# Optimization experiments

Measured on AMD Instinct MI355X. Metric: run time of the kernel, lower is better.

## Reference

```python
import jax, jax.numpy as jnp
import numpy as np

B, H, W, C = 32, 56, 56, 256
HEADS, WS, SS, MLP = 8, 7, 3, 1024
N = WS * WS          # tokens per window = 49
HD = C // HEADS      # head dim = 32
SCALE = HD ** -0.5
EPS = 1e-5


def _rel_pos_index():
    coords = np.stack(np.meshgrid(np.arange(WS), np.arange(WS), indexing='ij')).reshape(2, -1)
    rel = (coords[:, :, None] - coords[:, None, :]).transpose(1, 2, 0)
    rel[:, :, 0] += WS - 1
    rel[:, :, 1] += WS - 1
    rel[:, :, 0] *= 2 * WS - 1
    return rel.sum(-1)  # (49, 49) int


def _shift_mask():
    ma = np.zeros((H, W), np.float32)
    sl = (slice(0, -WS), slice(-WS, -SS), slice(-SS, None))
    cnt = 0
    for hs in sl:
        for ws_ in sl:
            ma[hs, ws_] = cnt
            cnt += 1
    mw = ma.reshape(H // WS, WS, W // WS, WS).transpose(0, 2, 1, 3).reshape(-1, N)
    diff = mw[:, None, :] - mw[:, :, None]
    return np.where(diff != 0, np.float32(-100.0), np.float32(0.0))  # (nW, 49, 49)


_RPI = _rel_pos_index()
_MASK = jnp.asarray(_shift_mask())


def _ln(x, g, b):
    mu = jnp.mean(x, -1, keepdims=True)
    var = jnp.mean(jnp.square(x - mu), -1, keepdims=True)
    return (x - mu) * jax.lax.rsqrt(var + EPS) * g + b


def setup_inputs() -> dict:
    key = jax.random.key(0)
    ks = jax.random.split(key, 6)
    s = 0.02
    return {
        'x': jax.random.normal(ks[0], (B, H * W, C), jnp.float32),
        'qkv_w': jax.random.normal(ks[1], (C, 3 * C), jnp.float32) * s,
        'qkv_b': jnp.zeros((3 * C,), jnp.float32),
        'proj_w': jax.random.normal(ks[2], (C, C), jnp.float32) * s,
        'proj_b': jnp.zeros((C,), jnp.float32),
        'rel_bias': jax.random.normal(ks[3], ((2 * WS - 1) ** 2, HEADS), jnp.float32) * s,
        'ln1_g': jnp.ones((C,), jnp.float32),
        'ln1_b': jnp.zeros((C,), jnp.float32),
        'ln2_g': jnp.ones((C,), jnp.float32),
        'ln2_b': jnp.zeros((C,), jnp.float32),
        'mlp_w1': jax.random.normal(ks[4], (C, MLP), jnp.float32) * s,
        'mlp_b1': jnp.zeros((MLP,), jnp.float32),
        'mlp_w2': jax.random.normal(ks[5], (MLP, C), jnp.float32) * s,
        'mlp_b2': jnp.zeros((C,), jnp.float32),
    }


def reference(x, qkv_w, qkv_b, proj_w, proj_b, rel_bias,
              ln1_g, ln1_b, ln2_g, ln2_b, mlp_w1, mlp_b1, mlp_w2, mlp_b2):
    b = x.shape[0]
    nW = (H // WS) * (W // WS)

    x_skip = x
    xn = _ln(x, ln1_g, ln1_b).reshape(b, H, W, C)
    shifted = jnp.roll(xn, (-SS, -SS), axis=(1, 2))
    # window partition -> (b*nW, N, C)
    xw = shifted.reshape(b, H // WS, WS, W // WS, WS, C)
    xw = xw.transpose(0, 1, 3, 2, 4, 5).reshape(-1, N, C)

    qkv = (xw @ qkv_w + qkv_b).reshape(-1, N, 3, HEADS, HD).transpose(2, 0, 3, 1, 4)
    q, k, v = qkv[0] * SCALE, qkv[1], qkv[2]  # (b*nW, heads, N, hd)

    attn = jnp.einsum('bhnd,bhmd->bhnm', q, k)
    bias = rel_bias[_RPI.reshape(-1)].reshape(N, N, HEADS).transpose(2, 0, 1)
    attn = attn + bias[None]
    attn = attn.reshape(b, nW, HEADS, N, N) + _MASK[None, :, None]
    attn = jax.nn.softmax(attn.reshape(-1, HEADS, N, N), axis=-1)

    out = jnp.einsum('bhnm,bhmd->bhnd', attn, v)
    out = out.transpose(0, 2, 1, 3).reshape(-1, N, C)
    out = out @ proj_w + proj_b

    # window reverse -> (b, H, W, C)
    out = out.reshape(b, H // WS, W // WS, WS, WS, C)
    out = out.transpose(0, 1, 3, 2, 4, 5).reshape(b, H, W, C)
    out = jnp.roll(out, (SS, SS), axis=(1, 2)).reshape(b, H * W, C)

    x = x_skip + out
    x_skip2 = x
    xn2 = _ln(x, ln2_g, ln2_b)
    h = jax.nn.gelu(xn2 @ mlp_w1 + mlp_b1, approximate=False)
    h = h @ mlp_w2 + mlp_b2
    return x_skip2 + h
```

## Files before the change

### kernel.cpp

```cpp
#include <hip/hip_runtime.h>


typedef unsigned short u16;
typedef __attribute__((ext_vector_type(8))) short bfrag8;
typedef __attribute__((ext_vector_type(8))) unsigned short u16x8;
typedef __attribute__((ext_vector_type(4))) float f32x4;

#define WS_TOK 49
#define C_DIM 256
#define M_ROWS 100352
#define N_WIN 2048
#define SCALE_Q 0.17677669529663689f

#if defined(__has_builtin)
#  if __has_builtin(__builtin_amdgcn_global_load_lds)
#    define HAVE_GLL 1
#  endif
#endif
#ifndef HAVE_GLL
#  define HAVE_GLL 0
#endif

__device__ __forceinline__ float u2f(u16 u) {
    union { unsigned int i; float f; } c; c.i = ((unsigned int)u) << 16; return c.f;
}
__device__ __forceinline__ u16 f2u(float f) {
    union { float f; unsigned int i; } c; c.f = f;
    unsigned int i = c.i;
    return (u16)((i + 0x7fffu + ((i >> 16) & 1u)) >> 16);
}
__device__ __forceinline__ int regionOf(int h) {
    return h < 49 ? 0 : (h < 53 ? 1 : 2);
}
__device__ __forceinline__ float gelu_fast(float v) {
    const float v2 = v * v;
    const float u = v * __builtin_fmaf(-0.0713548162f, v2, -1.5957691216f);
    const float e = __expf(u);
    return v * __builtin_amdgcn_rcpf(1.f + e);
}

__device__ __forceinline__ void g2l16(const u16* g, u16* l) {
#if HAVE_GLL
    __builtin_amdgcn_global_load_lds((const __attribute__((address_space(1))) void*)g,
                                     (__attribute__((address_space(3))) void*)l, 16, 0, 0);
#else
    *(bfrag8*)l = *(const bfrag8*)g;
#endif
}

__global__ void transpose_k(const float* __restrict__ in, u16* __restrict__ out,
                            int R, int Ccols) {
    int i = blockIdx.x * 256 + threadIdx.x;
    if (i < R * Ccols) {
        int r = i / Ccols, c = i - r * Ccols;
        out[(size_t)c * R + r] = f2u(in[i]);
    }
}

__global__ __launch_bounds__(256) void ln_kernel(const float* __restrict__ xin,
                                                 const float* __restrict__ g,
                                                 const float* __restrict__ b,
                                                 u16* __restrict__ out, int mode) {
    const int w = threadIdx.x >> 6, lane = threadIdx.x & 63;
    const int r = blockIdx.x * 4 + w;
    int s = r;
    if (mode == 0) {
        const int win = r / WS_TOK, tok = r - win * WS_TOK;
        const int b_ = win >> 6, w64 = win & 63;
        const int wr = w64 >> 3, wc = w64 & 7;
        const int th = tok / 7, tw = tok - th * 7;
        int hh = wr * 7 + th + 3; if (hh >= 56) hh -= 56;
        int ww = wc * 7 + tw + 3; if (ww >= 56) ww -= 56;
        s = b_ * 3136 + hh * 56 + ww;
    }
    const float4 u = *(const float4*)(xin + (size_t)s * C_DIM + lane * 4);
    float f0 = u.x, f1 = u.y, f2 = u.z, f3 = u.w;
    float s1 = f0 + f1 + f2 + f3;
    float s2 = f0 * f0 + f1 * f1 + f2 * f2 + f3 * f3;
#pragma unroll
    for (int off = 32; off; off >>= 1) {
        s1 += __shfl_xor(s1, off, 64);
        s2 += __shfl_xor(s2, off, 64);
    }
    const float mu = s1 * (1.f / 256.f);
    const float rs = rsqrtf(s2 * (1.f / 256.f) - mu * mu + 1e-5f);
    const float4 ug = *(const float4*)(g + lane * 4);
    const float4 ub = *(const float4*)(b + lane * 4);
    ushort4 o;
    o.x = f2u((f0 - mu) * rs * ug.x + ub.x);
    o.y = f2u((f1 - mu) * rs * ug.y + ub.y);
    o.z = f2u((f2 - mu) * rs * ug.z + ub.z);
    o.w = f2u((f3 - mu) * rs * ug.w + ub.w);
    *(ushort4*)(out + (size_t)r * C_DIM + lane * 4) = o;
}

template <int KD, int ND, int NY, int EPI>
__global__ __launch_bounds__(256) void gemm_bt(const u16* __restrict__ A,
                                               const u16* __restrict__ Bt,
                                               const float* __restrict__ bias,
                                               u16* __restrict__ o0,
                                               u16* __restrict__ o1,
                                               u16* __restrict__ o2,
                                               float* __restrict__ fo,
                                               const float* __restrict__ res) {
    __shared__ __align__(16) char pool[17408];
    u16* As = (u16*)pool;
    u16* Bs = (u16*)(pool + 8192);
    const int tid = threadIdx.x;
    const int bid = blockIdx.x;
    const int m0 = (bid / NY) * 128;
    const int n0 = (bid % NY) * 128;
    const int wid = tid >> 6, lane = tid & 63;
    const int wy = wid >> 1, wx = wid & 1;
    const int l15 = lane & 15, lsel = lane >> 4;

    f32x4 acc[4][4] = {};
    const u16* Ag = A + (size_t)m0 * KD;
    const u16* Bg = Bt + (size_t)n0 * KD;

    for (int k0 = 0; k0 < KD; k0 += 32) {
#pragma unroll
        for (int p = 0; p < 2; ++p) {
            const int idx = p * 256 + tid;
            const int row = idx >> 2, ks = (idx & 3) << 3;
            g2l16(Ag + (size_t)row * KD + k0 + ks, As + idx * 8);
            g2l16(Bg + (size_t)row * KD + k0 + ks, Bs + idx * 8);
        }
        __syncthreads();
        bfrag8 af[4], bfv[4];
#pragma unroll
        for (int m = 0; m < 4; ++m)
            af[m] = *(const bfrag8*)(As + (wy * 64 + m * 16 + l15) * 32 + lsel * 8);
#pragma unroll
        for (int n = 0; n < 4; ++n)
            bfv[n] = *(const bfrag8*)(Bs + (wx * 64 + n * 16 + l15) * 32 + lsel * 8);
#pragma unroll
        for (int m = 0; m < 4; ++m)
#pragma unroll
            for (int n = 0; n < 4; ++n)
                acc[m][n] = __builtin_amdgcn_mfma_f32_16x16x32_bf16(af[m], bfv[n],
                                                                    acc[m][n], 0, 0, 0);
        __syncthreads();
    }

    float* Ts = (float*)pool + wid * (16 * 68);
    const int r  = lane >> 2;
    const int cg = (lane & 3) << 4;

#pragma unroll
    for (int m = 0; m < 4; ++m) {
#pragma unroll
        for (int n = 0; n < 4; ++n)
#pragma unroll
            for (int reg = 0; reg < 4; ++reg)
                Ts[(lsel * 4 + reg) * 68 + n * 16 + l15] = acc[m][n][reg];
        float vals[16];
#pragma unroll
        for (int j = 0; j < 4; ++j)
            *(f32x4*)(vals + 4 * j) = *(const f32x4*)(Ts + r * 68 + cg + 4 * j);

        const int gr  = m0 + wy * 64 + m * 16 + r;
        const int gc0 = n0 + wx * 64 + cg;
        float bias16[16];
#pragma unroll
        for (int j = 0; j < 4; ++j)
            *(f32x4*)(bias16 + 4 * j) = *(const f32x4*)(bias + gc0 + 4 * j);

        if (EPI == 0) {
            const int win = gr / WS_TOK, tok = gr - win * WS_TOK;
            const int part = gc0 >> 8, head = (gc0 >> 5) & 7, hd = gc0 & 31;
            u16* dst = (part == 0) ? o0 : (part == 1) ? o1 : o2;
            const float sc = (part == 0) ? SCALE_Q : 1.f;
            const size_t di = (size_t)win * 8 * (WS_TOK * 32) + (size_t)tok * 32 +
                              (size_t)head * (WS_TOK * 32) + hd;
            u16x8 pk[2];
#pragma unroll
            for (int j = 0; j < 16; ++j)
                ((u16*)pk)[j] = f2u((vals[j] + bias16[j]) * sc);
            *(u16x8*)(dst + di)     = pk[0];
            *(u16x8*)(dst + di + 8) = pk[1];
        } else if (EPI == 1) {
            const int win = gr / WS_TOK, tok = gr - win * WS_TOK;
            const int b_ = win >> 6, w64 = win & 63;
            const int wr = w64 >> 3, wc = w64 & 7;
            const int th = tok / 7, tw = tok - th * 7;
            int hh = wr * 7 + th + 3; if (hh >= 56) hh -= 56;
            int ww = wc * 7 + tw + 3; if (ww >= 56) ww -= 56;
            const size_t di = ((size_t)b_ * 3136 + hh * 56 + ww) * C_DIM + gc0;
#pragma unroll
            for (int j = 0; j < 4; ++j) {
                f32x4 rr = *(const f32x4*)(res + di + 4 * j);
                f32x4 o;
#pragma unroll
                for (int e = 0; e < 4; ++e)
                    o[e] = rr[e] + vals[4 * j + e] + bias16[4 * j + e];
                *(f32x4*)(fo + di + 4 * j) = o;
            }
        } else if (EPI == 2) {
            u16x8 pk[2];
#pragma unroll
            for (int j = 0; j < 16; ++j)
                ((u16*)pk)[j] = f2u(gelu_fast(vals[j] + bias16[j]));
            u16* dst = o0 + (size_t)gr * ND + gc0;
            *(u16x8*)dst       = pk[0];
            *(u16x8*)(dst + 8) = pk[1];
        } else {
            const size_t di = (size_t)gr * ND + gc0;
#pragma unroll
            for (int j = 0; j < 4; ++j) {
                f32x4 rr = *(const f32x4*)(res + di + 4 * j);
                f32x4 o;
#pragma unroll
                for (int e = 0; e < 4; ++e)
                    o[e] = rr[e] + vals[4 * j + e] + bias16[4 * j + e];
                *(f32x4*)(fo + di + 4 * j) = o;
            }
        }
    }
}

__device__ __forceinline__ void stage_w1t(const u16* __restrict__ w1T, u16* dst,
                                          int kc, int k0, int tid) {
#pragma unroll
    for (int p = 0; p < 4; ++p) {
        const int i = p * 256 + tid;
        const int row = i >> 3, s = i & 7;
        g2l16(w1T + (size_t)(kc * 128 + row) * 256 + k0 + ((s ^ (row & 7)) << 3),
              dst + i * 8);
    }
}
__device__ __forceinline__ void stage_w2t(const u16* __restrict__ w2T, u16* dst,
                                          int kc, int bs, int tid) {
#pragma unroll
    for (int p = 0; p < 4; ++p) {
        const int i = p * 256 + tid;
        const int row = i >> 2, s = i & 3;
        g2l16(w2T + (size_t)row * 1024 + kc * 128 + bs * 32 +
                  ((s ^ ((row >> 1) & 3)) << 3),
              dst + i * 8);
    }
}

__global__ __launch_bounds__(256, 2) void fused_mlp(const u16* __restrict__ z,
                                                    const u16* __restrict__ w1T,
                                                    const float* __restrict__ b1,
                                                    const u16* __restrict__ w2T,
                                                    const float* __restrict__ b2,
                                                    float* __restrict__ out) {
    __shared__ __align__(16) u16 pool[40960];
    u16* zS  = pool;
    u16* wb0 = pool + 16384;
    u16* wb1 = pool + 24576;
    u16* hc  = pool + 32768;
    const int tid = threadIdx.x;
    const int wid = tid >> 6, lane = tid & 63;
    const int wy = wid >> 1, wx = wid & 1;
    const int l15 = lane & 15, lsel = lane >> 4;
    const int m0 = blockIdx.x * 64;

#pragma unroll
    for (int p = 0; p < 8; ++p) {
        const int i = p * 256 + tid;
        const int row = i >> 5, s = i & 31;
        g2l16(z + (size_t)(m0 + row) * 256 + ((s ^ (row & 7)) << 3), zS + i * 8);
    }
    stage_w1t(w1T, wb0, 0, 0, tid);

    f32x4 acc2[2][8] = {};

    for (int kc = 0; kc < 8; ++kc) {
        float b1v[4];
#pragma unroll
        for (int n = 0; n < 4; ++n)
            b1v[n] = b1[kc * 128 + wx * 64 + n * 16 + l15];
        asm volatile("" ::: "memory");

        f32x4 acc1[2][4] = {};
#pragma unroll
        for (int ks = 0; ks < 4; ++ks) {
            u16* wc = (ks & 1) ? wb1 : wb0;
            u16* wn = (ks & 1) ? wb0 : wb1;
            if (ks < 3) stage_w1t(w1T, wn, kc, (ks + 1) * 64, tid);
            else        stage_w2t(w2T, wn, kc, 0, tid);
            asm volatile("s_waitcnt vmcnt(4)" ::: "memory");
            __builtin_amdgcn_sched_barrier(0);
            __builtin_amdgcn_s_barrier();
            bfrag8 af[2], bf[4];
#pragma unroll
            for (int m = 0; m < 2; ++m) {
                const int r = wy * 32 + m * 16 + l15;
                af[m] = *(const bfrag8*)(zS + r * 256 +
                         ((ks * 64 + lsel * 8) ^ ((r & 7) << 3)));
            }
#pragma unroll
            for (int n = 0; n < 4; ++n) {
                const int r = wx * 64 + n * 16 + l15;
                bf[n] = *(const bfrag8*)(wc + r * 64 +
                         ((lsel * 8) ^ ((r & 7) << 3)));
            }
            bfrag8 af2[2], bf2[4];
#pragma unroll
            for (int m = 0; m < 2; ++m) {
                const int r = wy * 32 + m * 16 + l15;
                af2[m] = *(const bfrag8*)(zS + r * 256 +
                          ((ks * 64 + 32 + lsel * 8) ^ ((r & 7) << 3)));
            }
#pragma unroll
            for (int n = 0; n < 4; ++n) {
                const int r = wx * 64 + n * 16 + l15;
                bf2[n] = *(const bfrag8*)(wc + r * 64 +
                          ((32 + lsel * 8) ^ ((r & 7) << 3)));
            }
            __builtin_amdgcn_s_setprio(1);
#pragma unroll
            for (int m = 0; m < 2; ++m)
#pragma unroll
                for (int n = 0; n < 4; ++n)
                    acc1[m][n] = __builtin_amdgcn_mfma_f32_16x16x32_bf16(
                        af[m], bf[n], acc1[m][n], 0, 0, 0);
#pragma unroll
            for (int m = 0; m < 2; ++m)
#pragma unroll
                for (int n = 0; n < 4; ++n)
                    acc1[m][n] = __builtin_amdgcn_mfma_f32_16x16x32_bf16(
                        af2[m], bf2[n], acc1[m][n], 0, 0, 0);
            __builtin_amdgcn_s_setprio(0);
            if (ks == 3) {
#pragma unroll
                for (int m = 0; m < 2; ++m)
#pragma unroll
                    for (int n = 0; n < 4; ++n)
#pragma unroll
                        for (int reg = 0; reg < 4; ++reg) {
                            const int rh = wy * 32 + m * 16 + lsel * 4 + reg;
                            const int ch = wx * 64 + n * 16 + l15;
                            hc[rh * 128 + (ch ^ ((rh & 15) << 3))] =
                                f2u(gelu_fast(acc1[m][n][reg] + b1v[n]));
                        }
                asm volatile("s_waitcnt lgkmcnt(0)" ::: "memory");
                __builtin_amdgcn_sched_barrier(0);
            }
            __builtin_amdgcn_s_barrier();
        }
#pragma unroll
        for (int bs = 0; bs < 4; ++bs) {
            u16* wc = (bs & 1) ? wb1 : wb0;
            u16* wn = (bs & 1) ? wb0 : wb1;
            if (bs < 3)      stage_w2t(w2T, wn, kc, bs + 1, tid);
            else if (kc < 7) stage_w1t(w1T, wn, kc + 1, 0, tid);
            if (bs == 3 && kc == 7) asm volatile("s_waitcnt vmcnt(0)" ::: "memory");
            else                    asm volatile("s_waitcnt vmcnt(4)" ::: "memory");
            __builtin_amdgcn_sched_barrier(0);
            __builtin_amdgcn_s_barrier();
            bfrag8 a2[2], bb[8];
#pragma unroll
            for (int m = 0; m < 2; ++m) {
                const int r = wy * 32 + m * 16 + l15;
                a2[m] = *(const bfrag8*)(hc + r * 128 +
                         ((bs * 32 + lsel * 8) ^ ((r & 15) << 3)));
            }
#pragma unroll
            for (int n = 0; n < 8; ++n) {
                const int r = wx * 128 + n * 16 + l15;
                bb[n] = *(const bfrag8*)(wc + r * 32 +
                         ((lsel * 8) ^ (((r >> 1) & 3) << 3)));
            }
            __builtin_amdgcn_s_setprio(1);
#pragma unroll
            for (int m = 0; m < 2; ++m)
#pragma unroll
                for (int n = 0; n < 8; ++n)
                    acc2[m][n] = __builtin_amdgcn_mfma_f32_16x16x32_bf16(
                        a2[m], bb[n], acc2[m][n], 0, 0, 0);
            __builtin_amdgcn_s_setprio(0);
            __builtin_amdgcn_s_barrier();
        }
    }

    float* Ts = (float*)pool + wid * (16 * 132);
    const int r  = lane >> 2;
    const int cg = (lane & 3) << 5;
#pragma unroll
    for (int m = 0; m < 2; ++m) {
#pragma unroll
        for (int n = 0; n < 8; ++n)
#pragma unroll
            for (int reg = 0; reg < 4; ++reg)
                Ts[(lsel * 4 + reg) * 132 + n * 16 + l15] = acc2[m][n][reg];
        float vals[32];
#pragma unroll
        for (int j = 0; j < 8; ++j)
            *(f32x4*)(vals + 4 * j) = *(const f32x4*)(Ts + r * 132 + cg + 4 * j);

        const int gr = m0 + wy * 32 + m * 16 + r;
        const size_t dbase = (size_t)gr * 256 + wx * 128 + cg;
#pragma unroll
        for (int j = 0; j < 8; ++j) {
            f32x4 rr = *(const f32x4*)(out + dbase + 4 * j);
            f32x4 bb4 = *(const f32x4*)(b2 + wx * 128 + cg + 4 * j);
            f32x4 o;
#pragma unroll
            for (int e = 0; e < 4; ++e)
                o[e] = rr[e] + vals[4 * j + e] + bb4[e];
            *(f32x4*)(out + dbase + 4 * j) = o;
        }
    }
}

__global__ __launch_bounds__(256) void attn_kernel(const u16* __restrict__ q,
                                                   const u16* __restrict__ k,
                                                   const u16* __restrict__ v,
                                                   const float* __restrict__ relb,
                                                   u16* __restrict__ ao) {
    __shared__ __align__(16) u16 PbAll[4][64 * 64];
    __shared__ __align__(16) u16 VtAll[4][32 * 64];
    const int wid = threadIdx.x >> 6;
    const int lane = threadIdx.x & 63;
    u16* Pb = PbAll[wid];
    u16* Vt = VtAll[wid];
    const int bid = blockIdx.x * 4 + wid;
    const int head = bid & 7, win = bid >> 3;
    const int w64 = win & 63;
    const int wr = w64 >> 3, wc = w64 & 7;
    const int l15 = lane & 15, lsel = lane >> 4;
    const size_t base = (size_t)bid * (WS_TOK * 32);
    const u16* qb = q + base;
    const u16* kb = k + base;
    const u16* vb = v + base;

    for (int idx = lane; idx < WS_TOK * 32; idx += 64) {
        const int tok = idx >> 5, dim = idx & 31;
        Vt[dim * 64 + tok] = vb[idx];
    }
    for (int i = lane; i < 32 * 15; i += 64) {
        const int dim = i / 15, tok = 49 + (i - dim * 15);
        Vt[dim * 64 + tok] = 0;
    }

    bfrag8 qf[4], kf[4];
#pragma unroll
    for (int m = 0; m < 4; ++m) {
        int tok = m * 16 + l15; if (tok > 48) tok = 48;
        qf[m] = *(const bfrag8*)(qb + tok * 32 + lsel * 8);
    }
#pragma unroll
    for (int n = 0; n < 4; ++n) {
        int tok = n * 16 + l15; if (tok > 48) tok = 48;
        kf[n] = *(const bfrag8*)(kb + tok * 32 + lsel * 8);
    }
    f32x4 S[4][4] = {};
#pragma unroll
    for (int m = 0; m < 4; ++m)
#pragma unroll
        for (int n = 0; n < 4; ++n)
            S[m][n] = __builtin_amdgcn_mfma_f32_16x16x32_bf16(qf[m], kf[n], S[m][n], 0, 0, 0);

#pragma unroll
    for (int m = 0; m < 4; ++m) {
#pragma unroll
        for (int reg = 0; reg < 4; ++reg) {
            const int row = m * 16 + lsel * 4 + reg;
            const int rowc = row > 48 ? 48 : row;
            const int ih = rowc / 7, iw = rowc - ih * 7;
            const int ri = regionOf(wr * 7 + ih) * 3 + regionOf(wc * 7 + iw);
            float sv[4];
#pragma unroll
            for (int n = 0; n < 4; ++n) {
                const int col = n * 16 + l15;
                float val = S[m][n][reg];
                if (col > 48) {
                    val = -1e30f;
                } else {
                    const int jh = col / 7, jw = col - jh * 7;
                    val += relb[((ih - jh + 6) * 13 + (iw - jw + 6)) * 8 + head];
                    const int rj = regionOf(wr * 7 + jh) * 3 + regionOf(wc * 7 + jw);
                    if (ri != rj) val -= 100.f;
                }
                sv[n] = val;
            }
            float mx = fmaxf(fmaxf(sv[0], sv[1]), fmaxf(sv[2], sv[3]));
#pragma unroll
            for (int off = 1; off < 16; off <<= 1) mx = fmaxf(mx, __shfl_xor(mx, off, 64));
            float p[4], sum = 0.f;
#pragma unroll
            for (int n = 0; n < 4; ++n) { p[n] = __expf(sv[n] - mx); sum += p[n]; }
#pragma unroll
            for (int off = 1; off < 16; off <<= 1) sum += __shfl_xor(sum, off, 64);
            const float inv = 1.f / sum;
#pragma unroll
            for (int n = 0; n < 4; ++n)
                Pb[row * 64 + n * 16 + l15] = f2u(p[n] * inv);
        }
    }

    f32x4 O[4][2] = {};
    bfrag8 vf[2][2];
#pragma unroll
    for (int n = 0; n < 2; ++n) {
        vf[n][0] = *(const bfrag8*)(Vt + (n * 16 + l15) * 64 + lsel * 8);
        vf[n][1] = *(const bfrag8*)(Vt + (n * 16 + l15) * 64 + 32 + lsel * 8);
    }
#pragma unroll
    for (int m = 0; m < 4; ++m) {
        const bfrag8 pf0 = *(const bfrag8*)(Pb + (m * 16 + l15) * 64 + lsel * 8);
        const bfrag8 pf1 = *(const bfrag8*)(Pb + (m * 16 + l15) * 64 + 32 + lsel * 8);
#pragma unroll
        for (int n = 0; n < 2; ++n) {
            O[m][n] = __builtin_amdgcn_mfma_f32_16x16x32_bf16(pf0, vf[n][0], O[m][n], 0, 0, 0);
            O[m][n] = __builtin_amdgcn_mfma_f32_16x16x32_bf16(pf1, vf[n][1], O[m][n], 0, 0, 0);
        }
    }
    const size_t aob = (size_t)win * (WS_TOK * C_DIM) + head * 32;
#pragma unroll
    for (int m = 0; m < 4; ++m) {
#pragma unroll
        for (int reg = 0; reg < 4; ++reg) {
            const int row = m * 16 + lsel * 4 + reg;
            if (row < WS_TOK) {
#pragma unroll
                for (int n = 0; n < 2; ++n)
                    ao[aob + (size_t)row * C_DIM + n * 16 + l15] = f2u(O[m][n][reg]);
            }
        }
    }
}

extern "C" void kernel_launch(void* const* d_in, const int* in_sizes, int n_in,
                              void* d_out, int out_size, void* d_ws, size_t ws_size,
                              hipStream_t stream) {
    (void)in_sizes; (void)n_in; (void)out_size; (void)ws_size;
    const float* x      = (const float*)d_in[0];
    const float* qkv_w  = (const float*)d_in[1];
    const float* qkv_b  = (const float*)d_in[2];
    const float* proj_w = (const float*)d_in[3];
    const float* proj_b = (const float*)d_in[4];
    const float* relb   = (const float*)d_in[5];
    const float* ln1g   = (const float*)d_in[6];
    const float* ln1b   = (const float*)d_in[7];
    const float* ln2g   = (const float*)d_in[8];
    const float* ln2b   = (const float*)d_in[9];
    const float* w1     = (const float*)d_in[10];
    const float* b1     = (const float*)d_in[11];
    const float* w2     = (const float*)d_in[12];
    const float* b2     = (const float*)d_in[13];
    float* out = (float*)d_out;

    const size_t SZ = (size_t)M_ROWS * C_DIM;
    u16* wsu  = (u16*)d_ws;
    u16* xw   = wsu;
    u16* qq   = wsu + SZ;
    u16* kk   = wsu + 2 * SZ;
    u16* vv   = wsu + 3 * SZ;
    u16* ao   = wsu + 4 * SZ;
    u16* z    = xw;
    u16* qkvT = wsu + 5 * SZ;
    u16* projT = qkvT + 256 * 768;
    u16* w1T  = projT + 256 * 256;
    u16* w2T  = w1T + 256 * 1024;

    transpose_k<<<768, 256, 0, stream>>>(qkv_w, qkvT, 256, 768);
    transpose_k<<<256, 256, 0, stream>>>(proj_w, projT, 256, 256);
    transpose_k<<<1024, 256, 0, stream>>>(w1, w1T, 256, 1024);
    transpose_k<<<1024, 256, 0, stream>>>(w2, w2T, 1024, 256);

    ln_kernel<<<M_ROWS / 4, 256, 0, stream>>>(x, ln1g, ln1b, xw, 0);

    gemm_bt<256, 768, 6, 0><<<784 * 6, 256, 0, stream>>>(xw, qkvT, qkv_b,
                                                         qq, kk, vv, nullptr, nullptr);

    attn_kernel<<<N_WIN * 8 / 4, 256, 0, stream>>>(qq, kk, vv, relb, ao);

    gemm_bt<256, 256, 2, 1><<<784 * 2, 256, 0, stream>>>(ao, projT, proj_b,
                                                         nullptr, nullptr, nullptr, out, x);

    ln_kernel<<<M_ROWS / 4, 256, 0, stream>>>(out, ln2g, ln2b, z, 1);

    fused_mlp<<<M_ROWS / 64, 256, 0, stream>>>(z, w1T, b1, w2T, b2, out);
}
```

Measured before the change: 724.3 us.

## Double the fused MLP row tile to 128 and quad-buffer weight staging

The fused MLP kernel now runs 512-thread blocks, each covering 128 rows instead of 64, so every staged W1/W2 weight tile is reused by twice as many rows. Weight staging moves from two buffers to four, so loads are issued further ahead, with the vmcnt waits and the b1 prefetch rescheduled to match. The epilogue is also reorganised so each lane handles one float4 per row when adding bias and residual. The cost is LDS use of about 160KB per block, which allows only one block per CU and makes the hand-tuned wait counts harder to keep correct.

```diff
diff --git a/kernel.cpp b/kernel.cpp
--- a/kernel.cpp
+++ b/kernel.cpp
@@ -220,20 +220,20 @@
 }
 
 __device__ __forceinline__ void stage_w1t(const u16* __restrict__ w1T, u16* dst,
-                                          int kc, int k0, int tid) {
-#pragma unroll
-    for (int p = 0; p < 4; ++p) {
-        const int i = p * 256 + tid;
+                                          int kc, int ks, int tid) {
+#pragma unroll
+    for (int p = 0; p < 2; ++p) {
+        const int i = p * 512 + tid;
         const int row = i >> 3, s = i & 7;
-        g2l16(w1T + (size_t)(kc * 128 + row) * 256 + k0 + ((s ^ (row & 7)) << 3),
+        g2l16(w1T + (size_t)(kc * 128 + row) * 256 + ks * 64 + ((s ^ (row & 7)) << 3),
               dst + i * 8);
     }
 }
 __device__ __forceinline__ void stage_w2t(const u16* __restrict__ w2T, u16* dst,
                                           int kc, int bs, int tid) {
 #pragma unroll
-    for (int p = 0; p < 4; ++p) {
-        const int i = p * 256 + tid;
+    for (int p = 0; p < 2; ++p) {
+        const int i = p * 512 + tid;
         const int row = i >> 2, s = i & 3;
         g2l16(w2T + (size_t)row * 1024 + kc * 128 + bs * 32 +
                   ((s ^ ((row >> 1) & 3)) << 3),
@@ -241,73 +241,68 @@
     }
 }
 
-__global__ __launch_bounds__(256, 2) void fused_mlp(const u16* __restrict__ z,
+__global__ __launch_bounds__(512, 2) void fused_mlp(const u16* __restrict__ z,
                                                     const u16* __restrict__ w1T,
                                                     const float* __restrict__ b1,
                                                     const u16* __restrict__ w2T,
                                                     const float* __restrict__ b2,
                                                     float* __restrict__ out) {
-    __shared__ __align__(16) u16 pool[40960];
+    __shared__ __align__(16) u16 pool[81920];
     u16* zS  = pool;
-    u16* wb0 = pool + 16384;
-    u16* wb1 = pool + 24576;
-    u16* hc  = pool + 32768;
+    u16* wb[4] = { pool + 32768, pool + 40960, pool + 49152, pool + 57344 };
+    u16* hc  = pool + 65536;
     const int tid = threadIdx.x;
     const int wid = tid >> 6, lane = tid & 63;
     const int wy = wid >> 1, wx = wid & 1;
     const int l15 = lane & 15, lsel = lane >> 4;
-    const int m0 = blockIdx.x * 64;
+    const int m0 = blockIdx.x * 128;
 
 #pragma unroll
     for (int p = 0; p < 8; ++p) {
-        const int i = p * 256 + tid;
+        const int i = p * 512 + tid;
         const int row = i >> 5, s = i & 31;
         g2l16(z + (size_t)(m0 + row) * 256 + ((s ^ (row & 7)) << 3), zS + i * 8);
     }
-    stage_w1t(w1T, wb0, 0, 0, tid);
+    stage_w1t(w1T, wb[0], 0, 0, tid);
+    stage_w1t(w1T, wb[1], 0, 1, tid);
+    stage_w1t(w1T, wb[2], 0, 2, tid);
+    asm volatile("" ::: "memory");
+    float b1v[4];
+#pragma unroll
+    for (int n = 0; n < 4; ++n)
+        b1v[n] = b1[wx * 64 + n * 16 + l15];
+    asm volatile("" ::: "memory");
 
     f32x4 acc2[2][8] = {};
 
     for (int kc = 0; kc < 8; ++kc) {
-        float b1v[4];
-#pragma unroll
-        for (int n = 0; n < 4; ++n)
-            b1v[n] = b1[kc * 128 + wx * 64 + n * 16 + l15];
-        asm volatile("" ::: "memory");
-
         f32x4 acc1[2][4] = {};
 #pragma unroll
         for (int ks = 0; ks < 4; ++ks) {
-            u16* wc = (ks & 1) ? wb1 : wb0;
-            u16* wn = (ks & 1) ? wb0 : wb1;
-            if (ks < 3) stage_w1t(w1T, wn, kc, (ks + 1) * 64, tid);
-            else        stage_w2t(w2T, wn, kc, 0, tid);
-            asm volatile("s_waitcnt vmcnt(4)" ::: "memory");
+            u16* wc = wb[ks];
+            if (ks == 0)      stage_w1t(w1T, wb[3], kc, 3, tid);
+            else if (ks == 1) stage_w2t(w2T, wb[0], kc, 0, tid);
+            else if (ks == 2) stage_w2t(w2T, wb[1], kc, 1, tid);
+            else              stage_w2t(w2T, wb[2], kc, 2, tid);
+            if (ks < 2) asm volatile("s_waitcnt vmcnt(10)" ::: "memory");
+            else        asm volatile("s_waitcnt vmcnt(6)"  ::: "memory");
             __builtin_amdgcn_sched_barrier(0);
             __builtin_amdgcn_s_barrier();
-            bfrag8 af[2], bf[4];
+            __builtin_amdgcn_sched_barrier(0);
+            bfrag8 af[2], bf[4], af2[2], bf2[4];
 #pragma unroll
             for (int m = 0; m < 2; ++m) {
                 const int r = wy * 32 + m * 16 + l15;
-                af[m] = *(const bfrag8*)(zS + r * 256 +
-                         ((ks * 64 + lsel * 8) ^ ((r & 7) << 3)));
+                af[m]  = *(const bfrag8*)(zS + r * 256 +
+                          ((ks * 64 + lsel * 8) ^ ((r & 7) << 3)));
+                af2[m] = *(const bfrag8*)(zS + r * 256 +
+                          ((ks * 64 + 32 + lsel * 8) ^ ((r & 7) << 3)));
             }
 #pragma unroll
             for (int n = 0; n < 4; ++n) {
                 const int r = wx * 64 + n * 16 + l15;
-                bf[n] = *(const bfrag8*)(wc + r * 64 +
-                         ((lsel * 8) ^ ((r & 7) << 3)));
-            }
-            bfrag8 af2[2], bf2[4];
-#pragma unroll
-            for (int m = 0; m < 2; ++m) {
-                const int r = wy * 32 + m * 16 + l15;
-                af2[m] = *(const bfrag8*)(zS + r * 256 +
-                          ((ks * 64 + 32 + lsel * 8) ^ ((r & 7) << 3)));
-            }
-#pragma unroll
-            for (int n = 0; n < 4; ++n) {
-                const int r = wx * 64 + n * 16 + l15;
+                bf[n]  = *(const bfrag8*)(wc + r * 64 +
+                          ((lsel * 8) ^ ((r & 7) << 3)));
                 bf2[n] = *(const bfrag8*)(wc + r * 64 +
                           ((32 + lsel * 8) ^ ((r & 7) << 3)));
             }
@@ -344,14 +339,32 @@
         }
 #pragma unroll
         for (int bs = 0; bs < 4; ++bs) {
-            u16* wc = (bs & 1) ? wb1 : wb0;
-            u16* wn = (bs & 1) ? wb0 : wb1;
-            if (bs < 3)      stage_w2t(w2T, wn, kc, bs + 1, tid);
-            else if (kc < 7) stage_w1t(w1T, wn, kc + 1, 0, tid);
-            if (bs == 3 && kc == 7) asm volatile("s_waitcnt vmcnt(0)" ::: "memory");
-            else                    asm volatile("s_waitcnt vmcnt(4)" ::: "memory");
+            u16* wc = wb[bs];
+            if (bs == 0) stage_w2t(w2T, wb[3], kc, 3, tid);
+            else if (kc < 7) {
+                if (bs == 1)      stage_w1t(w1T, wb[0], kc + 1, 0, tid);
+                else if (bs == 2) stage_w1t(w1T, wb[1], kc + 1, 1, tid);
+                else              stage_w1t(w1T, wb[2], kc + 1, 2, tid);
+            }
+            if (bs == 3 && kc < 7) {
+                asm volatile("" ::: "memory");
+#pragma unroll
+                for (int n = 0; n < 4; ++n)
+                    b1v[n] = b1[(kc + 1) * 128 + wx * 64 + n * 16 + l15];
+                asm volatile("" ::: "memory");
+            }
+            if (bs == 0)            asm volatile("s_waitcnt vmcnt(6)"  ::: "memory");
+            else if (kc < 7) {
+                if (bs < 3)         asm volatile("s_waitcnt vmcnt(6)"  ::: "memory");
+                else                asm volatile("s_waitcnt vmcnt(10)" ::: "memory");
+            } else {
+                if (bs == 1)        asm volatile("s_waitcnt vmcnt(4)"  ::: "memory");
+                else if (bs == 2)   asm volatile("s_waitcnt vmcnt(2)"  ::: "memory");
+                else                asm volatile("s_waitcnt vmcnt(0)"  ::: "memory");
+            }
             __builtin_amdgcn_sched_barrier(0);
             __builtin_amdgcn_s_barrier();
+            __builtin_amdgcn_sched_barrier(0);
             bfrag8 a2[2], bb[8];
 #pragma unroll
             for (int m = 0; m < 2; ++m) {
@@ -378,8 +391,8 @@
     }
 
     float* Ts = (float*)pool + wid * (16 * 132);
-    const int r  = lane >> 2;
-    const int cg = (lane & 3) << 5;
+    const int hrow = lane >> 5;
+    const int c4   = (lane & 31) << 2;
 #pragma unroll
     for (int m = 0; m < 2; ++m) {
 #pragma unroll
@@ -387,22 +400,19 @@
 #pragma unroll
             for (int reg = 0; reg < 4; ++reg)
                 Ts[(lsel * 4 + reg) * 132 + n * 16 + l15] = acc2[m][n][reg];
-        float vals[32];
-#pragma unroll
-        for (int j = 0; j < 8; ++j)
-            *(f32x4*)(vals + 4 * j) = *(const f32x4*)(Ts + r * 132 + cg + 4 * j);
-
-        const int gr = m0 + wy * 32 + m * 16 + r;
-        const size_t dbase = (size_t)gr * 256 + wx * 128 + cg;
 #pragma unroll
         for (int j = 0; j < 8; ++j) {
-            f32x4 rr = *(const f32x4*)(out + dbase + 4 * j);
-            f32x4 bb4 = *(const f32x4*)(b2 + wx * 128 + cg + 4 * j);
+            const int lrow = j * 2 + hrow;
+            f32x4 v = *(const f32x4*)(Ts + lrow * 132 + c4);
+            const int gr = m0 + wy * 32 + m * 16 + lrow;
+            const size_t di = (size_t)gr * 256 + wx * 128 + c4;
+            f32x4 rr  = *(const f32x4*)(out + di);
+            f32x4 bb4 = *(const f32x4*)(b2 + wx * 128 + c4);
             f32x4 o;
 #pragma unroll
             for (int e = 0; e < 4; ++e)
-                o[e] = rr[e] + vals[4 * j + e] + bb4[e];
-            *(f32x4*)(out + dbase + 4 * j) = o;
+                o[e] = rr[e] + v[e] + bb4[e];
+            *(f32x4*)(out + di) = o;
         }
     }
 }
@@ -575,5 +585,5 @@
 
     ln_kernel<<<M_ROWS / 4, 256, 0, stream>>>(out, ln2g, ln2b, z, 1);
 
-    fused_mlp<<<M_ROWS / 64, 256, 0, stream>>>(z, w1T, b1, w2T, b2, out);
-}
+    fused_mlp<<<M_ROWS / 128, 512, 0, stream>>>(z, w1T, b1, w2T, b2, out);
+}
```

Result: no change. 738.4 us (+2.0%).

## Enlarge fused MLP tile to 128 rows with 512 threads, load z directly

Applied to the files above, without the earlier changes.

The fused MLP kernel now processes 128 rows per block with 8 waves in a 2x4 layout instead of 64 rows with 4 waves, and hidden chunks grow from 128 to 256 columns. Weight traffic per row is halved because each staged weight tile serves twice as many rows. The z activations are no longer staged in LDS but loaded straight from global memory into registers each k-step, and the W1/W2 staging is unified into one helper. LDS use rises to 128 KB per block and register pressure grows with 4x4 accumulator tiles, which may limit occupancy.

```diff
diff --git a/kernel.cpp b/kernel.cpp
--- a/kernel.cpp
+++ b/kernel.cpp
@@ -219,122 +219,92 @@
     }
 }
 
-__device__ __forceinline__ void stage_w1t(const u16* __restrict__ w1T, u16* dst,
-                                          int kc, int k0, int tid) {
+__device__ __forceinline__ void stage32(const u16* __restrict__ base, int rstride,
+                                        u16* dst, int tid) {
 #pragma unroll
     for (int p = 0; p < 4; ++p) {
-        const int i = p * 256 + tid;
+        const int i = p * 512 + tid;
         const int row = i >> 3, s = i & 7;
-        g2l16(w1T + (size_t)(kc * 128 + row) * 256 + k0 + ((s ^ (row & 7)) << 3),
-              dst + i * 8);
-    }
-}
-__device__ __forceinline__ void stage_w2t(const u16* __restrict__ w2T, u16* dst,
-                                          int kc, int bs, int tid) {
-#pragma unroll
-    for (int p = 0; p < 4; ++p) {
-        const int i = p * 256 + tid;
-        const int row = i >> 2, s = i & 3;
-        g2l16(w2T + (size_t)row * 1024 + kc * 128 + bs * 32 +
-                  ((s ^ ((row >> 1) & 3)) << 3),
-              dst + i * 8);
-    }
-}
-
-__global__ __launch_bounds__(256, 2) void fused_mlp(const u16* __restrict__ z,
+        g2l16(base + (size_t)row * rstride + ((s ^ (row & 7)) << 3), dst + i * 8);
+    }
+}
+
+__global__ __launch_bounds__(512, 2) void fused_mlp(const u16* __restrict__ z,
                                                     const u16* __restrict__ w1T,
                                                     const float* __restrict__ b1,
                                                     const u16* __restrict__ w2T,
                                                     const float* __restrict__ b2,
                                                     float* __restrict__ out) {
-    __shared__ __align__(16) u16 pool[40960];
-    u16* zS  = pool;
-    u16* wb0 = pool + 16384;
-    u16* wb1 = pool + 24576;
-    u16* hc  = pool + 32768;
+    __shared__ __align__(16) u16 pool[65536];
+    u16* hc  = pool;
+    u16* sb0 = pool + 32768;
+    u16* sb1 = pool + 49152;
     const int tid = threadIdx.x;
     const int wid = tid >> 6, lane = tid & 63;
-    const int wy = wid >> 1, wx = wid & 1;
+    const int wy = wid >> 2, wx = wid & 3;
     const int l15 = lane & 15, lsel = lane >> 4;
-    const int m0 = blockIdx.x * 64;
-
-#pragma unroll
-    for (int p = 0; p < 8; ++p) {
-        const int i = p * 256 + tid;
-        const int row = i >> 5, s = i & 31;
-        g2l16(z + (size_t)(m0 + row) * 256 + ((s ^ (row & 7)) << 3), zS + i * 8);
-    }
-    stage_w1t(w1T, wb0, 0, 0, tid);
-
-    f32x4 acc2[2][8] = {};
-
-    for (int kc = 0; kc < 8; ++kc) {
+    const int m0 = blockIdx.x * 128;
+
+    stage32(w1T, 256, sb0, tid);
+
+    f32x4 acc2[4][4] = {};
+
+#pragma unroll 1
+    for (int kc = 0; kc < 4; ++kc) {
         float b1v[4];
 #pragma unroll
         for (int n = 0; n < 4; ++n)
-            b1v[n] = b1[kc * 128 + wx * 64 + n * 16 + l15];
+            b1v[n] = b1[kc * 256 + wx * 64 + n * 16 + l15];
         asm volatile("" ::: "memory");
 
-        f32x4 acc1[2][4] = {};
+        f32x4 acc1[4][4] = {};
 #pragma unroll
         for (int ks = 0; ks < 4; ++ks) {
-            u16* wc = (ks & 1) ? wb1 : wb0;
-            u16* wn = (ks & 1) ? wb0 : wb1;
-            if (ks < 3) stage_w1t(w1T, wn, kc, (ks + 1) * 64, tid);
-            else        stage_w2t(w2T, wn, kc, 0, tid);
-            asm volatile("s_waitcnt vmcnt(4)" ::: "memory");
+            bfrag8 zf[4][2];
+#pragma unroll
+            for (int m = 0; m < 4; ++m)
+#pragma unroll
+                for (int kh = 0; kh < 2; ++kh)
+                    zf[m][kh] = *(const bfrag8*)(z +
+                        (size_t)(m0 + wy * 64 + m * 16 + l15) * 256 +
+                        ks * 64 + kh * 32 + lsel * 8);
+            if (ks < 3) stage32(w1T + (size_t)(kc * 256) * 256 + (ks + 1) * 64,
+                                256, (ks & 1) ? sb0 : sb1, tid);
+            else        stage32(w2T + (size_t)kc * 256, 1024, sb0, tid);
+            asm volatile("s_waitcnt vmcnt(12)" ::: "memory");
             __builtin_amdgcn_sched_barrier(0);
             __builtin_amdgcn_s_barrier();
-            bfrag8 af[2], bf[4];
-#pragma unroll
-            for (int m = 0; m < 2; ++m) {
-                const int r = wy * 32 + m * 16 + l15;
-                af[m] = *(const bfrag8*)(zS + r * 256 +
-                         ((ks * 64 + lsel * 8) ^ ((r & 7) << 3)));
-            }
+            __builtin_amdgcn_sched_barrier(0);
+            const u16* cur = (ks & 1) ? sb1 : sb0;
+            bfrag8 bf[4][2];
 #pragma unroll
             for (int n = 0; n < 4; ++n) {
                 const int r = wx * 64 + n * 16 + l15;
-                bf[n] = *(const bfrag8*)(wc + r * 64 +
-                         ((lsel * 8) ^ ((r & 7) << 3)));
-            }
-            bfrag8 af2[2], bf2[4];
-#pragma unroll
-            for (int m = 0; m < 2; ++m) {
-                const int r = wy * 32 + m * 16 + l15;
-                af2[m] = *(const bfrag8*)(zS + r * 256 +
-                          ((ks * 64 + 32 + lsel * 8) ^ ((r & 7) << 3)));
-            }
-#pragma unroll
-            for (int n = 0; n < 4; ++n) {
-                const int r = wx * 64 + n * 16 + l15;
-                bf2[n] = *(const bfrag8*)(wc + r * 64 +
-                          ((32 + lsel * 8) ^ ((r & 7) << 3)));
+#pragma unroll
+                for (int kh = 0; kh < 2; ++kh)
+                    bf[n][kh] = *(const bfrag8*)(cur + r * 64 +
+                                 ((kh * 32 + lsel * 8) ^ ((r & 7) << 3)));
             }
             __builtin_amdgcn_s_setprio(1);
 #pragma unroll
-            for (int m = 0; m < 2; ++m)
-#pragma unroll
-                for (int n = 0; n < 4; ++n)
-                    acc1[m][n] = __builtin_amdgcn_mfma_f32_16x16x32_bf16(
-                        af[m], bf[n], acc1[m][n], 0, 0, 0);
-#pragma unroll
-            for (int m = 0; m < 2; ++m)
-#pragma unroll
-                for (int n = 0; n < 4; ++n)
-                    acc1[m][n] = __builtin_amdgcn_mfma_f32_16x16x32_bf16(
-                        af2[m], bf2[n], acc1[m][n], 0, 0, 0);
+            for (int kh = 0; kh < 2; ++kh)
+#pragma unroll
+                for (int m = 0; m < 4; ++m)
+#pragma unroll
+                    for (int n = 0; n < 4; ++n)
+                        acc1[m][n] = __builtin_amdgcn_mfma_f32_16x16x32_bf16(
+                            zf[m][kh], bf[n][kh], acc1[m][n], 0, 0, 0);
             __builtin_amdgcn_s_setprio(0);
             if (ks == 3) {
 #pragma unroll
-                for (int m = 0; m < 2; ++m)
+                for (int m = 0; m < 4; ++m)
 #pragma unroll
                     for (int n = 0; n < 4; ++n)
 #pragma unroll
                         for (int reg = 0; reg < 4; ++reg) {
-                            const int rh = wy * 32 + m * 16 + lsel * 4 + reg;
+                            const int rh = wy * 64 + m * 16 + lsel * 4 + reg;
                             const int ch = wx * 64 + n * 16 + l15;
-                            hc[rh * 128 + (ch ^ ((rh & 15) << 3))] =
+                            hc[rh * 256 + (ch ^ ((rh & 15) << 3))] =
                                 f2u(gelu_fast(acc1[m][n][reg] + b1v[n]));
                         }
                 asm volatile("s_waitcnt lgkmcnt(0)" ::: "memory");
@@ -344,65 +314,76 @@
         }
 #pragma unroll
         for (int bs = 0; bs < 4; ++bs) {
-            u16* wc = (bs & 1) ? wb1 : wb0;
-            u16* wn = (bs & 1) ? wb0 : wb1;
-            if (bs < 3)      stage_w2t(w2T, wn, kc, bs + 1, tid);
-            else if (kc < 7) stage_w1t(w1T, wn, kc + 1, 0, tid);
-            if (bs == 3 && kc == 7) asm volatile("s_waitcnt vmcnt(0)" ::: "memory");
-            else                    asm volatile("s_waitcnt vmcnt(4)" ::: "memory");
+            if (bs < 3)
+                stage32(w2T + (size_t)kc * 256 + (bs + 1) * 64, 1024,
+                        (bs & 1) ? sb0 : sb1, tid);
+            else if (kc < 3)
+                stage32(w1T + (size_t)((kc + 1) * 256) * 256, 256, sb0, tid);
+            if (bs == 3 && kc == 3) {
+                asm volatile("s_waitcnt vmcnt(0)" ::: "memory");
+            } else {
+                asm volatile("s_waitcnt vmcnt(4)" ::: "memory");
+            }
             __builtin_amdgcn_sched_barrier(0);
             __builtin_amdgcn_s_barrier();
-            bfrag8 a2[2], bb[8];
-#pragma unroll
-            for (int m = 0; m < 2; ++m) {
-                const int r = wy * 32 + m * 16 + l15;
-                a2[m] = *(const bfrag8*)(hc + r * 128 +
-                         ((bs * 32 + lsel * 8) ^ ((r & 15) << 3)));
-            }
-#pragma unroll
-            for (int n = 0; n < 8; ++n) {
-                const int r = wx * 128 + n * 16 + l15;
-                bb[n] = *(const bfrag8*)(wc + r * 32 +
-                         ((lsel * 8) ^ (((r >> 1) & 3) << 3)));
+            __builtin_amdgcn_sched_barrier(0);
+            const u16* cur = (bs & 1) ? sb1 : sb0;
+            bfrag8 a2[4][2], bb[4][2];
+#pragma unroll
+            for (int m = 0; m < 4; ++m) {
+                const int r = wy * 64 + m * 16 + l15;
+#pragma unroll
+                for (int kh = 0; kh < 2; ++kh)
+                    a2[m][kh] = *(const bfrag8*)(hc + r * 256 +
+                        ((bs * 64 + kh * 32 + lsel * 8) ^ ((r & 15) << 3)));
+            }
+#pragma unroll
+            for (int n = 0; n < 4; ++n) {
+                const int r = wx * 64 + n * 16 + l15;
+#pragma unroll
+                for (int kh = 0; kh < 2; ++kh)
+                    bb[n][kh] = *(const bfrag8*)(cur + r * 64 +
+                                 ((kh * 32 + lsel * 8) ^ ((r & 7) << 3)));
             }
             __builtin_amdgcn_s_setprio(1);
 #pragma unroll
-            for (int m = 0; m < 2; ++m)
-#pragma unroll
-                for (int n = 0; n < 8; ++n)
-                    acc2[m][n] = __builtin_amdgcn_mfma_f32_16x16x32_bf16(
-                        a2[m], bb[n], acc2[m][n], 0, 0, 0);
+            for (int kh = 0; kh < 2; ++kh)
+#pragma unroll
+                for (int m = 0; m < 4; ++m)
+#pragma unroll
+                    for (int n = 0; n < 4; ++n)
+                        acc2[m][n] = __builtin_amdgcn_mfma_f32_16x16x32_bf16(
+                            a2[m][kh], bb[n][kh], acc2[m][n], 0, 0, 0);
             __builtin_amdgcn_s_setprio(0);
             __builtin_amdgcn_s_barrier();
         }
     }
 
-    float* Ts = (float*)pool + wid * (16 * 132);
-    const int r  = lane >> 2;
-    const int cg = (lane & 3) << 5;
-#pragma unroll
-    for (int m = 0; m < 2; ++m) {
-#pragma unroll
-        for (int n = 0; n < 8; ++n)
+    float* Ts = (float*)pool + wid * (16 * 68);
+    const int r_ = lane >> 2;
+    const int cg = (lane & 3) << 4;
+#pragma unroll
+    for (int m = 0; m < 4; ++m) {
+#pragma unroll
+        for (int n = 0; n < 4; ++n)
 #pragma unroll
             for (int reg = 0; reg < 4; ++reg)
-                Ts[(lsel * 4 + reg) * 132 + n * 16 + l15] = acc2[m][n][reg];
-        float vals[32];
-#pragma unroll
-        for (int j = 0; j < 8; ++j)
-            *(f32x4*)(vals + 4 * j) = *(const f32x4*)(Ts + r * 132 + cg + 4 * j);
-
-        const int gr = m0 + wy * 32 + m * 16 + r;
-        const size_t dbase = (size_t)gr * 256 + wx * 128 + cg;
-#pragma unroll
-        for (int j = 0; j < 8; ++j) {
-            f32x4 rr = *(const f32x4*)(out + dbase + 4 * j);
-            f32x4 bb4 = *(const f32x4*)(b2 + wx * 128 + cg + 4 * j);
+                Ts[(lsel * 4 + reg) * 68 + n * 16 + l15] = acc2[m][n][reg];
+        float vals[16];
+#pragma unroll
+        for (int j = 0; j < 4; ++j)
+            *(f32x4*)(vals + 4 * j) = *(const f32x4*)(Ts + r_ * 68 + cg + 4 * j);
+        const int gr = m0 + wy * 64 + m * 16 + r_;
+        const size_t di = (size_t)gr * 256 + wx * 64 + cg;
+#pragma unroll
+        for (int j = 0; j < 4; ++j) {
+            f32x4 rr  = *(const f32x4*)(out + di + 4 * j);
+            f32x4 bb4 = *(const f32x4*)(b2 + wx * 64 + cg + 4 * j);
             f32x4 o;
 #pragma unroll
             for (int e = 0; e < 4; ++e)
                 o[e] = rr[e] + vals[4 * j + e] + bb4[e];
-            *(f32x4*)(out + dbase + 4 * j) = o;
+            *(f32x4*)(out + di + 4 * j) = o;
         }
     }
 }
@@ -575,5 +556,5 @@
 
     ln_kernel<<<M_ROWS / 4, 256, 0, stream>>>(out, ln2g, ln2b, z, 1);
 
-    fused_mlp<<<M_ROWS / 64, 256, 0, stream>>>(z, w1T, b1, w2T, b2, out);
-}
+    fused_mlp<<<M_ROWS / 128, 512, 0, stream>>>(z, w1T, b1, w2T, b2, out);
+}
```

Measured after the change: 1.049 ms. +44.8%, slower.
